# Kernel optimization log

Measured on AMD Instinct MI355X. Metric: run time of the kernel, lower is better.

## Reference

```python
import jax, jax.numpy as jnp
import numpy as np

N_USERS = 100_000
N_ENTITIES = 400_000
N_NODES = N_USERS + N_ENTITIES  # 500k
DIM = 64
N_EDGES = 2_000_000
BATCH = 4096
N_LAYERS = 3
CF_WEIGHT = 1.0
L2_REG = 1e-4


def setup_inputs() -> dict:
    key = jax.random.key(0)
    k_emb, k_e, k_u, k_p, k_n = jax.random.split(key, 5)
    # xavier_uniform on (N, D): bound = sqrt(6/(N+D))
    bound = float(np.sqrt(6.0 / (N_NODES + DIM)))
    emb = jax.random.uniform(k_emb, (N_NODES, DIM), jnp.float32, -bound, bound)
    edge_index = jax.random.randint(k_e, (2, N_EDGES), 0, N_NODES, dtype=jnp.int32)
    user_idx = jax.random.randint(k_u, (BATCH,), 0, N_USERS, dtype=jnp.int32)
    pos_item = jax.random.randint(k_p, (BATCH,), 0, N_NODES, dtype=jnp.int32)
    neg_item = jax.random.randint(k_n, (BATCH,), 0, N_NODES, dtype=jnp.int32)
    return {"emb": emb, "edge_index": edge_index, "user_idx": user_idx,
            "pos_item": pos_item, "neg_item": neg_item}


def _lightgcn(emb, edge_index, n_layers):
    # LGConv(normalize=True): x' = D^{-1/2} A D^{-1/2} x, no self loops.
    n = emb.shape[0]
    src, dst = edge_index[0], edge_index[1]
    deg = jax.ops.segment_sum(jnp.ones_like(dst, dtype=emb.dtype), dst,
                              num_segments=n)
    dinv = jnp.where(deg > 0, jax.lax.rsqrt(jnp.maximum(deg, 1e-12)), 0.0)
    norm = dinv[src] * dinv[dst]  # [E]
    x = emb
    acc = emb  # layer-0 term of the mean over stacked layers
    for _ in range(n_layers):
        msgs = x[src] * norm[:, None]  # [E, D] gather + scale
        x = jax.ops.segment_sum(msgs, dst, num_segments=n)  # scatter-add
        acc = acc + x
    return acc / (n_layers + 1)  # mean over (layers+1) stacked embeddings


def reference(emb, edge_index, user_idx, pos_item, neg_item):
    all_layer = _lightgcn(emb, edge_index, N_LAYERS)
    u = all_layer[user_idx]
    p = all_layer[pos_item]
    n_ = all_layer[neg_item]
    pos_score = jnp.sum(u * p, axis=-1)
    neg_score = jnp.sum(u * n_, axis=-1)
    # BPRLoss: -mean(logsigmoid(pos - neg)) == mean(softplus(neg - pos))
    cf_loss = jnp.mean(jax.nn.softplus(neg_score - pos_score))
    u_ego = emb[user_idx]
    p_ego = emb[pos_item]
    n_ego = emb[neg_item]
    reg_loss = 0.5 * (jnp.sum(u_ego ** 2) + jnp.sum(p_ego ** 2)
                      + jnp.sum(n_ego ** 2)) / float(BATCH)
    return CF_WEIGHT * cf_loss + L2_REG * reg_loss
```

## Files before the change

### kernel.cpp

```cpp
#include <hip/hip_runtime.h>
#include <cstdint>
#include <cstddef>

#define N_USERS   100000
#define N_NODES   500000
#define DIM       64
#define N_EDGES   2000000
#define BATCH     4096
#define SCAN_B    1024
#define NBLK      ((N_NODES + SCAN_B - 1) / SCAN_B)
#define X1C_CAP   280000
#define LA_CAP    100000
#define NXCD      8
#define EDG4_BLK  ((N_EDGES / 4 + 255) / 256)
#define CONV_BLK  ((N_NODES * 16 + 255) / 256)
#define CS_TOTAL  (EDG4_BLK * 17)
#define PROP_BLK  2048

typedef unsigned char uchar;
typedef unsigned short ushort;
typedef unsigned int uint;

__device__ __forceinline__ ushort f2bf(float f) {
    uint u = __float_as_uint(f);
    uint r = u + 0x7FFFu + ((u >> 16) & 1u);
    return (ushort)(r >> 16);
}
__device__ __forceinline__ float bflo(uint u) { return __uint_as_float(u << 16); }
__device__ __forceinline__ float bfhi(uint u) { return __uint_as_float(u & 0xFFFF0000u); }

__device__ __forceinline__ uint xcc_id() {
    uint x;
    asm volatile("s_getreg_b32 %0, hwreg(HW_REG_XCC_ID)" : "=s"(x));
    return x & (NXCD - 1);
}

__global__ void k_mark(const int* __restrict__ u, const int* __restrict__ p,
                       const int* __restrict__ n, uchar* __restrict__ f3,
                       uchar* __restrict__ fA, uchar* __restrict__ fB) {
    int i = blockIdx.x * blockDim.x + threadIdx.x;
    if (i >= 3 * BATCH) return;
    int idx;
    if (i < BATCH)          idx = u[i];
    else if (i < 2 * BATCH) idx = p[i - BATCH];
    else                    idx = n[i - 2 * BATCH];
    f3[idx] = 1; fA[idx] = 1; fB[idx] = 1;
}

__global__ void k_deghist(const int* __restrict__ src, const int* __restrict__ dst,
                          int* __restrict__ degp, const uchar* __restrict__ f3,
                          uchar* __restrict__ fA) {
    int* mydeg = degp + (size_t)xcc_id() * N_NODES;
    int t = blockIdx.x * blockDim.x + threadIdx.x;
    if (t < N_EDGES / 4) {
        int4 s0 = ((const int4*)src)[t];
        int4 d0 = ((const int4*)dst)[t];
        __hip_atomic_fetch_add(&mydeg[d0.x], 1, __ATOMIC_RELAXED, __HIP_MEMORY_SCOPE_WORKGROUP);
        __hip_atomic_fetch_add(&mydeg[d0.y], 1, __ATOMIC_RELAXED, __HIP_MEMORY_SCOPE_WORKGROUP);
        __hip_atomic_fetch_add(&mydeg[d0.z], 1, __ATOMIC_RELAXED, __HIP_MEMORY_SCOPE_WORKGROUP);
        __hip_atomic_fetch_add(&mydeg[d0.w], 1, __ATOMIC_RELAXED, __HIP_MEMORY_SCOPE_WORKGROUP);
        if (f3[d0.x] && !fA[s0.x]) fA[s0.x] = 1;
        if (f3[d0.y] && !fA[s0.y]) fA[s0.y] = 1;
        if (f3[d0.z] && !fA[s0.z]) fA[s0.z] = 1;
        if (f3[d0.w] && !fA[s0.w]) fA[s0.w] = 1;
    }
}

__global__ void k_expand(const int* __restrict__ src, const int* __restrict__ dst,
                         const uchar* __restrict__ fin, uchar* __restrict__ fout) {
    int t = blockIdx.x * blockDim.x + threadIdx.x;
    if (t < N_EDGES / 4) {
        int4 s0 = ((const int4*)src)[t];
        int4 d0 = ((const int4*)dst)[t];
        if (fin[d0.x] && !fout[s0.x]) fout[s0.x] = 1;
        if (fin[d0.y] && !fout[s0.y]) fout[s0.y] = 1;
        if (fin[d0.z] && !fout[s0.z]) fout[s0.z] = 1;
        if (fin[d0.w] && !fout[s0.w]) fout[s0.w] = 1;
    }
}

__global__ void k_scanA(const int* __restrict__ degp, const uchar* __restrict__ fA,
                        const uchar* __restrict__ fB, int* __restrict__ degsum,
                        int* __restrict__ bsumD, int* __restrict__ bsumP) {
    __shared__ int sD[SCAN_B];
    __shared__ int sP[SCAN_B];
    int i = blockIdx.x * SCAN_B + threadIdx.x;
    int d = 0, pk = 0;
    if (i < N_NODES) {
        #pragma unroll
        for (int x = 0; x < NXCD; ++x) d += degp[(size_t)x * N_NODES + i];
        degsum[i] = d;
        pk = (int)fA[i] | ((int)fB[i] << 16);
    }
    sD[threadIdx.x] = d; sP[threadIdx.x] = pk;
    __syncthreads();
    for (int off = SCAN_B / 2; off; off >>= 1) {
        if (threadIdx.x < off) {
            sD[threadIdx.x] += sD[threadIdx.x + off];
            sP[threadIdx.x] += sP[threadIdx.x + off];
        }
        __syncthreads();
    }
    if (threadIdx.x == 0) { bsumD[blockIdx.x] = sD[0]; bsumP[blockIdx.x] = sP[0]; }
}

__global__ void k_scanB(const int* __restrict__ bsumD, const int* __restrict__ bsumP,
                        int* __restrict__ boffD, int* __restrict__ boffA,
                        int* __restrict__ boffB, int* __restrict__ counts) {
    __shared__ int sD[512];
    __shared__ int sA[512];
    __shared__ int sB[512];
    int d = (threadIdx.x < NBLK) ? bsumD[threadIdx.x] : 0;
    int p = (threadIdx.x < NBLK) ? bsumP[threadIdx.x] : 0;
    int a = p & 0xFFFF, b = p >> 16;
    sD[threadIdx.x] = d; sA[threadIdx.x] = a; sB[threadIdx.x] = b;
    __syncthreads();
    for (int off = 1; off < 512; off <<= 1) {
        int tD = (threadIdx.x >= off) ? sD[threadIdx.x - off] : 0;
        int tA = (threadIdx.x >= off) ? sA[threadIdx.x - off] : 0;
        int tB = (threadIdx.x >= off) ? sB[threadIdx.x - off] : 0;
        __syncthreads();
        sD[threadIdx.x] += tD; sA[threadIdx.x] += tA; sB[threadIdx.x] += tB;
        __syncthreads();
    }
    if (threadIdx.x < NBLK) {
        boffD[threadIdx.x] = sD[threadIdx.x] - d;
        boffA[threadIdx.x] = sA[threadIdx.x] - a;
        boffB[threadIdx.x] = sB[threadIdx.x] - b;
    }
    if (threadIdx.x == 511) { counts[0] = sA[511]; counts[1] = sB[511]; }
}

__global__ void k_scanC(const int* __restrict__ degsum, const uchar* __restrict__ fA,
                        const uchar* __restrict__ fB,
                        const int* __restrict__ boffD, const int* __restrict__ boffA,
                        const int* __restrict__ boffB,
                        int* __restrict__ rowstart, float* __restrict__ dinv,
                        int* __restrict__ mapA, int* __restrict__ mapB,
                        int4* __restrict__ listA4, int4* __restrict__ listB4) {
    __shared__ int sD[SCAN_B];
    __shared__ int sP[SCAN_B];
    int i = blockIdx.x * SCAN_B + threadIdx.x;
    int d = 0, a = 0, b = 0;
    if (i < N_NODES) { d = degsum[i]; a = (int)fA[i]; b = (int)fB[i]; }
    sD[threadIdx.x] = d; sP[threadIdx.x] = a | (b << 16);
    __syncthreads();
    for (int off = 1; off < SCAN_B; off <<= 1) {
        int tD = (threadIdx.x >= off) ? sD[threadIdx.x - off] : 0;
        int tP = (threadIdx.x >= off) ? sP[threadIdx.x - off] : 0;
        __syncthreads();
        sD[threadIdx.x] += tD; sP[threadIdx.x] += tP;
        __syncthreads();
    }
    if (i < N_NODES) {
        int exD = sD[threadIdx.x] - d + boffD[blockIdx.x];
        int incP = sP[threadIdx.x];
        int exA = (incP & 0xFFFF) - a + boffA[blockIdx.x];
        int exB = (incP >> 16) - b + boffB[blockIdx.x];
        rowstart[i] = exD;
        float dv = (d > 0) ? rsqrtf((float)d) : 0.0f;
        dinv[i] = dv;
        mapA[i] = a ? exA : -1;
        mapB[i] = b ? exB : -1;
        int4 ent = make_int4(exD, exD + d, __float_as_int(dv), 0);
        if (a) listA4[exA] = ent;
        if (b) listB4[exB] = ent;
    }
}

__global__ void k_convscatter(const float* __restrict__ emb,
                              const float* __restrict__ dinv,
                              ushort* __restrict__ embs,
                              const int* __restrict__ src, const int* __restrict__ dst,
                              const uchar* __restrict__ fB,
                              int* __restrict__ rowstart, int* __restrict__ csr_src) {
    uint b = blockIdx.x;
    uint g = b / 17u;
    uint r = b - g * 17u;
    if (r == 8u) {
        int t = (int)g * blockDim.x + threadIdx.x;
        if (t < N_EDGES / 4) {
            int4 s0 = ((const int4*)src)[t];
            int4 d0 = ((const int4*)dst)[t];
            if (fB[d0.x]) csr_src[atomicAdd(&rowstart[d0.x], 1)] = s0.x;
            if (fB[d0.y]) csr_src[atomicAdd(&rowstart[d0.y], 1)] = s0.y;
            if (fB[d0.z]) csr_src[atomicAdd(&rowstart[d0.z], 1)] = s0.z;
            if (fB[d0.w]) csr_src[atomicAdd(&rowstart[d0.w], 1)] = s0.w;
        }
    } else {
        uint convblk = g * 16u + r - (r > 8u ? 1u : 0u);
        int c = (int)convblk * blockDim.x + threadIdx.x;
        if (c < N_NODES * 16) {
            int row = c >> 4;
            float4 v = ((const float4*)emb)[c];
            float dv = dinv[row];
            uint2 o;
            o.x = (uint)f2bf(v.x * dv) | ((uint)f2bf(v.y * dv) << 16);
            o.y = (uint)f2bf(v.z * dv) | ((uint)f2bf(v.w * dv) << 16);
            ((uint2*)embs)[c] = o;
        }
    }
}

__global__ void k_prop1(const ushort* __restrict__ embs, const int4* __restrict__ listB4,
                        const int* __restrict__ counts, const int* __restrict__ csr_src,
                        ushort* __restrict__ x1c) {
    int lane = threadIdx.x & 63;
    int sub = lane >> 4, q = lane & 15;
    int wv = (blockIdx.x * blockDim.x + threadIdx.x) >> 6;
    int nw = (gridDim.x * blockDim.x) >> 6;
    int cnt = counts[1];
    for (; wv < cnt; wv += nw) {
        int4 nb = listB4[wv];
        float4 acc = {0.f, 0.f, 0.f, 0.f};
        for (int i = nb.x + sub; i < nb.y; i += 4) {
            int s = csr_src[i];
            uint2 u = *(const uint2*)(embs + (size_t)s * DIM + q * 4);
            acc.x += bflo(u.x); acc.y += bfhi(u.x);
            acc.z += bflo(u.y); acc.w += bfhi(u.y);
        }
        for (int off = 16; off <= 32; off <<= 1) {
            acc.x += __shfl_xor(acc.x, off, 64);
            acc.y += __shfl_xor(acc.y, off, 64);
            acc.z += __shfl_xor(acc.z, off, 64);
            acc.w += __shfl_xor(acc.w, off, 64);
        }
        if (sub == 0) {
            float dv = __int_as_float(nb.z);
            float d2 = dv * dv;
            uint2 o;
            o.x = (uint)f2bf(acc.x * d2) | ((uint)f2bf(acc.y * d2) << 16);
            o.y = (uint)f2bf(acc.z * d2) | ((uint)f2bf(acc.w * d2) << 16);
            *(uint2*)(x1c + (size_t)wv * DIM + q * 4) = o;
        }
    }
}

__global__ void k_prop2(const ushort* __restrict__ x1c, const int* __restrict__ mapB,
                        const int4* __restrict__ listA4, const int* __restrict__ counts,
                        const int* __restrict__ csr_src, ushort* __restrict__ x2c) {
    int lane = threadIdx.x & 63;
    int sub = lane >> 4, q = lane & 15;
    int wv = (blockIdx.x * blockDim.x + threadIdx.x) >> 6;
    int nw = (gridDim.x * blockDim.x) >> 6;
    int cnt = counts[0];
    for (; wv < cnt; wv += nw) {
        int4 nb = listA4[wv];
        float4 acc = {0.f, 0.f, 0.f, 0.f};
        for (int i = nb.x + sub; i < nb.y; i += 4) {
            int s = csr_src[i];
            int slot = mapB[s];
            uint2 u = *(const uint2*)(x1c + (size_t)slot * DIM + q * 4);
            acc.x += bflo(u.x); acc.y += bfhi(u.x);
            acc.z += bflo(u.y); acc.w += bfhi(u.y);
        }
        for (int off = 16; off <= 32; off <<= 1) {
            acc.x += __shfl_xor(acc.x, off, 64);
            acc.y += __shfl_xor(acc.y, off, 64);
            acc.z += __shfl_xor(acc.z, off, 64);
            acc.w += __shfl_xor(acc.w, off, 64);
        }
        if (sub == 0) {
            float dv = __int_as_float(nb.z);
            float d2 = dv * dv;
            uint2 o;
            o.x = (uint)f2bf(acc.x * d2) | ((uint)f2bf(acc.y * d2) << 16);
            o.y = (uint)f2bf(acc.z * d2) | ((uint)f2bf(acc.w * d2) << 16);
            *(uint2*)(x2c + (size_t)wv * DIM + q * 4) = o;
        }
    }
}

__device__ __forceinline__ float x3_row(const ushort* __restrict__ x2c,
                                        const int* __restrict__ mapA,
                                        const int* __restrict__ csr_src,
                                        const int4* __restrict__ listB4,
                                        const int* __restrict__ mapB,
                                        int t, int lane) {
    int4 nb = listB4[mapB[t]];
    float acc = 0.f;
    for (int i = nb.x; i < nb.y; ++i) {
        int s = csr_src[i];
        int slot = mapA[s];
        acc += __uint_as_float((uint)x2c[(size_t)slot * DIM + lane] << 16);
    }
    return acc * __int_as_float(nb.z);
}

__global__ void k_loss(const float* __restrict__ emb, const ushort* __restrict__ x1c,
                       const ushort* __restrict__ x2c,
                       const int* __restrict__ mapA, const int* __restrict__ mapB,
                       const int4* __restrict__ listB4, const int* __restrict__ csr_src,
                       const float* __restrict__ dinv,
                       const int* __restrict__ u, const int* __restrict__ p,
                       const int* __restrict__ n, float* __restrict__ out) {
    int lane = threadIdx.x & 63;
    int w = (blockIdx.x * blockDim.x + threadIdx.x) >> 6;
    if (w >= BATCH) return;
    int ui = u[w], pi = p[w], ni = n[w];
    float dvu = dinv[ui], dvp = dinv[pi], dvn = dinv[ni];
    float rdu = dvu > 0.f ? 1.f / dvu : 0.f;
    float rdp = dvp > 0.f ? 1.f / dvp : 0.f;
    float rdn = dvn > 0.f ? 1.f / dvn : 0.f;
    float ue = emb[(size_t)ui * DIM + lane];
    float pe = emb[(size_t)pi * DIM + lane];
    float ne = emb[(size_t)ni * DIM + lane];
    float u1 = __uint_as_float((uint)x1c[(size_t)mapB[ui] * DIM + lane] << 16) * rdu;
    float p1 = __uint_as_float((uint)x1c[(size_t)mapB[pi] * DIM + lane] << 16) * rdp;
    float n1 = __uint_as_float((uint)x1c[(size_t)mapB[ni] * DIM + lane] << 16) * rdn;
    float u2 = __uint_as_float((uint)x2c[(size_t)mapA[ui] * DIM + lane] << 16) * rdu;
    float p2 = __uint_as_float((uint)x2c[(size_t)mapA[pi] * DIM + lane] << 16) * rdp;
    float n2 = __uint_as_float((uint)x2c[(size_t)mapA[ni] * DIM + lane] << 16) * rdn;
    float u3 = x3_row(x2c, mapA, csr_src, listB4, mapB, ui, lane);
    float p3 = x3_row(x2c, mapA, csr_src, listB4, mapB, pi, lane);
    float n3 = x3_row(x2c, mapA, csr_src, listB4, mapB, ni, lane);
    float uall = 0.25f * (ue + u1 + u2 + u3);
    float pall = 0.25f * (pe + p1 + p2 + p3);
    float nall = 0.25f * (ne + n1 + n2 + n3);
    float pos = uall * pall;
    float neg = uall * nall;
    float sq  = ue * ue + pe * pe + ne * ne;
    for (int off = 32; off; off >>= 1) {
        pos += __shfl_xor(pos, off, 64);
        neg += __shfl_xor(neg, off, 64);
        sq  += __shfl_xor(sq,  off, 64);
    }
    if (lane == 0) {
        float z = neg - pos;
        float sp = fmaxf(z, 0.0f) + log1pf(expf(-fabsf(z)));
        float contrib = sp * (1.0f / BATCH) + 1e-4f * 0.5f * sq * (1.0f / BATCH);
        atomicAdd(out, contrib);
    }
}

extern "C" void kernel_launch(void* const* d_in, const int* in_sizes, int n_in,
                              void* d_out, int out_size, void* d_ws, size_t ws_size,
                              hipStream_t stream) {
    const float* emb  = (const float*)d_in[0];
    const int*   edge = (const int*)d_in[1];
    const int*   src  = edge;
    const int*   dst  = edge + N_EDGES;
    const int*   uidx = (const int*)d_in[2];
    const int*   pidx = (const int*)d_in[3];
    const int*   nidx = (const int*)d_in[4];
    float* out = (float*)d_out;

    char* w = (char*)d_ws;
    ushort* embs    = (ushort*)w;                w += (size_t)N_NODES * DIM * 2;
    ushort* x1c     = (ushort*)w;                w += (size_t)X1C_CAP * DIM * 2;
    ushort* x2c     = (ushort*)w;                w += (size_t)LA_CAP * DIM * 2;
    float*  dinv    = (float*)w;                 w += (size_t)N_NODES * 4;
    int*    rowstart= (int*)w;                   w += (size_t)N_NODES * 4;
    int*    csr_src = (int*)w;                   w += (size_t)N_EDGES * 4;
    int*    mapA    = (int*)w;                   w += (size_t)N_NODES * 4;
    int*    mapB    = (int*)w;                   w += (size_t)N_NODES * 4;
    int*    degsum  = (int*)w;                   w += (size_t)N_NODES * 4;
    int4*   listA4  = (int4*)w;                  w += (size_t)LA_CAP * 16;
    int4*   listB4  = (int4*)w;                  w += (size_t)X1C_CAP * 16;
    char*   zbase   = w;
    int*    degp    = (int*)w;                   w += (size_t)NXCD * N_NODES * 4;
    uchar*  flags   = (uchar*)w;                 w += (size_t)3 * N_NODES;
    uchar*  f3 = flags;
    uchar*  fA = flags + N_NODES;
    uchar*  fB = flags + 2 * N_NODES;
    size_t  zbytes  = (size_t)(w - zbase);
    int*    bsumD   = (int*)w;                   w += (size_t)NBLK * 4;
    int*    boffD   = (int*)w;                   w += (size_t)NBLK * 4;
    int*    bsumP   = (int*)w;                   w += (size_t)NBLK * 4;
    int*    boffA   = (int*)w;                   w += (size_t)NBLK * 4;
    int*    boffB   = (int*)w;                   w += (size_t)NBLK * 4;
    int*    counts  = (int*)w;                   w += 16;

    hipMemsetAsync(zbase, 0, zbytes, stream);
    hipMemsetAsync(out, 0, 4, stream);

    k_mark<<<(3 * BATCH + 255) / 256, 256, 0, stream>>>(uidx, pidx, nidx, f3, fA, fB);

    k_deghist<<<EDG4_BLK, 256, 0, stream>>>(src, dst, degp, f3, fA);

    k_expand<<<EDG4_BLK, 256, 0, stream>>>(src, dst, fA, fB);

    k_scanA<<<NBLK, SCAN_B, 0, stream>>>(degp, fA, fB, degsum, bsumD, bsumP);
    k_scanB<<<1, 512, 0, stream>>>(bsumD, bsumP, boffD, boffA, boffB, counts);
    k_scanC<<<NBLK, SCAN_B, 0, stream>>>(degsum, fA, fB, boffD, boffA, boffB,
                                         rowstart, dinv, mapA, mapB, listA4, listB4);

    k_convscatter<<<CS_TOTAL, 256, 0, stream>>>(
        emb, dinv, embs, src, dst, fB, rowstart, csr_src);

    k_prop1<<<PROP_BLK, 256, 0, stream>>>(embs, listB4, counts, csr_src, x1c);
    k_prop2<<<PROP_BLK, 256, 0, stream>>>(x1c, mapB, listA4, counts, csr_src, x2c);

    k_loss<<<(BATCH * 64 + 255) / 256, 256, 0, stream>>>(
        emb, x1c, x2c, mapA, mapB, listB4, csr_src, dinv, uidx, pidx, nidx, out);
}
```

Before: 471.6 us.

## Replace global-atomic degree histogram with range-partitioned LDS histograms

The per-XCD global atomic degree histogram becomes 248 blocks. Each one owns a 16K-node range and one eighth of the edges, and counts degrees with packed 16-bit LDS atomics before writing its slice without atomics. The frontier-expansion work runs in extra blocks of the same launch. This removes scattered global atomics and the 16 MB zeroing of the per-XCD buffers. In exchange every histogram block rereads its whole edge slice (31x redundant dst reads), and the 16-bit counts rely on per-slice degrees staying under 65536.

New measurement: 486.8 us. 1.03x slower.

```diff
diff --git a/kernel.cpp b/kernel.cpp
--- a/kernel.cpp
+++ b/kernel.cpp
@@ -11,12 +11,19 @@
 #define NBLK      ((N_NODES + SCAN_B - 1) / SCAN_B)
 #define X1C_CAP   280000
 #define LA_CAP    100000
-#define NXCD      8
 #define EDG4_BLK  ((N_EDGES / 4 + 255) / 256)
 #define CONV_BLK  ((N_NODES * 16 + 255) / 256)
 #define CS_TOTAL  (EDG4_BLK * 17)
 #define PROP_BLK  2048
 
+#define RANGES    31
+#define RANGE_SZ  16384
+#define RANGE_TOT (RANGES * RANGE_SZ)
+#define HSLICES   8
+#define HIST_BLK  (RANGES * HSLICES)
+#define ESLICE    (N_EDGES / HSLICES)
+#define EINT4     (ESLICE / 4)
+
 typedef unsigned char uchar;
 typedef unsigned short ushort;
 typedef unsigned int uint;
@@ -28,12 +35,6 @@
 }
 __device__ __forceinline__ float bflo(uint u) { return __uint_as_float(u << 16); }
 __device__ __forceinline__ float bfhi(uint u) { return __uint_as_float(u & 0xFFFF0000u); }
-
-__device__ __forceinline__ uint xcc_id() {
-    uint x;
-    asm volatile("s_getreg_b32 %0, hwreg(HW_REG_XCC_ID)" : "=s"(x));
-    return x & (NXCD - 1);
-}
 
 __global__ void k_mark(const int* __restrict__ u, const int* __restrict__ p,
                        const int* __restrict__ n, uchar* __restrict__ f3,
@@ -47,22 +48,38 @@
     f3[idx] = 1; fA[idx] = 1; fB[idx] = 1;
 }
 
-__global__ void k_deghist(const int* __restrict__ src, const int* __restrict__ dst,
-                          int* __restrict__ degp, const uchar* __restrict__ f3,
+__global__ void k_histexp(const int* __restrict__ src, const int* __restrict__ dst,
+                          ushort* __restrict__ degp16, const uchar* __restrict__ f3,
                           uchar* __restrict__ fA) {
-    int* mydeg = degp + (size_t)xcc_id() * N_NODES;
-    int t = blockIdx.x * blockDim.x + threadIdx.x;
-    if (t < N_EDGES / 4) {
-        int4 s0 = ((const int4*)src)[t];
-        int4 d0 = ((const int4*)dst)[t];
-        __hip_atomic_fetch_add(&mydeg[d0.x], 1, __ATOMIC_RELAXED, __HIP_MEMORY_SCOPE_WORKGROUP);
-        __hip_atomic_fetch_add(&mydeg[d0.y], 1, __ATOMIC_RELAXED, __HIP_MEMORY_SCOPE_WORKGROUP);
-        __hip_atomic_fetch_add(&mydeg[d0.z], 1, __ATOMIC_RELAXED, __HIP_MEMORY_SCOPE_WORKGROUP);
-        __hip_atomic_fetch_add(&mydeg[d0.w], 1, __ATOMIC_RELAXED, __HIP_MEMORY_SCOPE_WORKGROUP);
-        if (f3[d0.x] && !fA[s0.x]) fA[s0.x] = 1;
-        if (f3[d0.y] && !fA[s0.y]) fA[s0.y] = 1;
-        if (f3[d0.z] && !fA[s0.z]) fA[s0.z] = 1;
-        if (f3[d0.w] && !fA[s0.w]) fA[s0.w] = 1;
+    __shared__ uint cnt[RANGE_SZ / 2];
+    if (blockIdx.x < HIST_BLK) {
+        int r = blockIdx.x >> 3;
+        int s = blockIdx.x & 7;
+        for (int k = threadIdx.x; k < RANGE_SZ / 2; k += 256) cnt[k] = 0;
+        __syncthreads();
+        int base = r * RANGE_SZ;
+        const int4* d4 = (const int4*)(dst + s * ESLICE);
+        for (int t = threadIdx.x; t < EINT4; t += 256) {
+            int4 d = d4[t];
+            int l;
+            l = d.x - base; if ((uint)l < RANGE_SZ) atomicAdd(&cnt[l >> 1], 1u << ((l & 1) << 4));
+            l = d.y - base; if ((uint)l < RANGE_SZ) atomicAdd(&cnt[l >> 1], 1u << ((l & 1) << 4));
+            l = d.z - base; if ((uint)l < RANGE_SZ) atomicAdd(&cnt[l >> 1], 1u << ((l & 1) << 4));
+            l = d.w - base; if ((uint)l < RANGE_SZ) atomicAdd(&cnt[l >> 1], 1u << ((l & 1) << 4));
+        }
+        __syncthreads();
+        uint* out = (uint*)degp16 + (size_t)s * (RANGE_TOT / 2) + r * (RANGE_SZ / 2);
+        for (int k = threadIdx.x; k < RANGE_SZ / 2; k += 256) out[k] = cnt[k];
+    } else {
+        int t = (blockIdx.x - HIST_BLK) * blockDim.x + threadIdx.x;
+        if (t < N_EDGES / 4) {
+            int4 s0 = ((const int4*)src)[t];
+            int4 d0 = ((const int4*)dst)[t];
+            if (f3[d0.x] && !fA[s0.x]) fA[s0.x] = 1;
+            if (f3[d0.y] && !fA[s0.y]) fA[s0.y] = 1;
+            if (f3[d0.z] && !fA[s0.z]) fA[s0.z] = 1;
+            if (f3[d0.w] && !fA[s0.w]) fA[s0.w] = 1;
+        }
     }
 }
 
@@ -79,7 +96,7 @@
     }
 }
 
-__global__ void k_scanA(const int* __restrict__ degp, const uchar* __restrict__ fA,
+__global__ void k_scanA(const ushort* __restrict__ degp16, const uchar* __restrict__ fA,
                         const uchar* __restrict__ fB, int* __restrict__ degsum,
                         int* __restrict__ bsumD, int* __restrict__ bsumP) {
     __shared__ int sD[SCAN_B];
@@ -88,7 +105,7 @@
     int d = 0, pk = 0;
     if (i < N_NODES) {
         #pragma unroll
-        for (int x = 0; x < NXCD; ++x) d += degp[(size_t)x * N_NODES + i];
+        for (int s = 0; s < HSLICES; ++s) d += (int)degp16[(size_t)s * RANGE_TOT + i];
         degsum[i] = d;
         pk = (int)fA[i] | ((int)fB[i] << 16);
     }
@@ -357,8 +374,8 @@
     int*    degsum  = (int*)w;                   w += (size_t)N_NODES * 4;
     int4*   listA4  = (int4*)w;                  w += (size_t)LA_CAP * 16;
     int4*   listB4  = (int4*)w;                  w += (size_t)X1C_CAP * 16;
+    ushort* degp16  = (ushort*)w;                w += (size_t)HSLICES * RANGE_TOT * 2;
     char*   zbase   = w;
-    int*    degp    = (int*)w;                   w += (size_t)NXCD * N_NODES * 4;
     uchar*  flags   = (uchar*)w;                 w += (size_t)3 * N_NODES;
     uchar*  f3 = flags;
     uchar*  fA = flags + N_NODES;
@@ -376,11 +393,11 @@
 
     k_mark<<<(3 * BATCH + 255) / 256, 256, 0, stream>>>(uidx, pidx, nidx, f3, fA, fB);
 
-    k_deghist<<<EDG4_BLK, 256, 0, stream>>>(src, dst, degp, f3, fA);
+    k_histexp<<<HIST_BLK + EDG4_BLK, 256, 0, stream>>>(src, dst, degp16, f3, fA);
 
     k_expand<<<EDG4_BLK, 256, 0, stream>>>(src, dst, fA, fB);
 
-    k_scanA<<<NBLK, SCAN_B, 0, stream>>>(degp, fA, fB, degsum, bsumD, bsumP);
+    k_scanA<<<NBLK, SCAN_B, 0, stream>>>(degp16, fA, fB, degsum, bsumD, bsumP);
     k_scanB<<<1, 512, 0, stream>>>(bsumD, bsumP, boffD, boffA, boffB, counts);
     k_scanC<<<NBLK, SCAN_B, 0, stream>>>(degsum, fA, fB, boffD, boffA, boffB,
                                          rowstart, dinv, mapA, mapB, listA4, listB4);
```
